# Kernel optimization log

Hardware: AMD Instinct MI355X
Metric: run time of the kernel (lower is better)

The kernel has to match this reference:

```python
import jax, jax.numpy as jnp
import numpy as np

NF, NH1, NH21, NH22, NCLS = 6, 128, 128, 128, 3
OBS_X, OBS_Y, OBS_Z, R = 10.0, 10.0, 9.0, 7.0
BATCH = 131072


def setup_inputs() -> dict:
    key = jax.random.key(0)
    ks = jax.random.split(key, 16)
    def lin(kw, kb, fan_in, fan_out):
        bound = 1.0 / np.sqrt(fan_in)
        w = jax.random.uniform(kw, (fan_out, fan_in), jnp.float32, -bound, bound)
        b = jax.random.uniform(kb, (fan_out,), jnp.float32, -bound, bound)
        return w, b
    fc1_w, fc1_b = lin(ks[0], ks[1], NF, NH1)
    fc21_w, fc21_b = lin(ks[2], ks[3], NH1, NH21)
    fc22_w, fc22_b = lin(ks[4], ks[5], NH1, NH22)
    fcm1_w, fcm1_b = lin(ks[6], ks[7], NH21, NH21)
    fcm2_w, fcm2_b = lin(ks[8], ks[9], NH22, NH22)
    fc31_w, fc31_b = lin(ks[10], ks[11], NH21, NCLS)
    fc32_w, fc32_b = lin(ks[12], ks[13], NH22, 2)
    x = jax.random.normal(ks[14], (BATCH, NF), jnp.float32)
    mean = jnp.array([10.0, 0.0, 10.0, 0.0, 9.0, 0.0], jnp.float32)
    std = jnp.array([5.0, 2.0, 5.0, 2.0, 5.0, 2.0], jnp.float32)
    return {"x": x, "mean": mean, "std": std,
            "fc1_w": fc1_w, "fc1_b": fc1_b,
            "fc21_w": fc21_w, "fc21_b": fc21_b,
            "fc22_w": fc22_w, "fc22_b": fc22_b,
            "fcm1_w": fcm1_w, "fcm1_b": fcm1_b,
            "fcm2_w": fcm2_w, "fcm2_b": fcm2_b,
            "fc31_w": fc31_w, "fc31_b": fc31_b,
            "fc32_w": fc32_w, "fc32_b": fc32_b,
            "sgn": 1}


def _forward(x, mean, std, fc1_w, fc1_b, fc21_w, fc21_b, fc22_w, fc22_b,
             fcm1_w, fcm1_b, fcm2_w, fcm2_b, fc31_w, fc31_b, fc32_w, fc32_b):
    x0 = x * std + mean                                   # de-normalized state [B,6]
    h = jnp.tanh(x @ fc1_w.T + fc1_b)                     # [B,NH1]
    x21 = jnp.tanh(h @ fc21_w.T + fc21_b)
    x22 = jnp.tanh(h @ fc22_w.T + fc22_b)
    x21 = jnp.tanh(x21 @ fcm1_w.T + fcm1_b)
    x22 = jnp.tanh(x22 @ fcm2_w.T + fcm2_b)
    x31 = x21 @ fc31_w.T + fc31_b                         # QP linear term p, [B,3]
    x32 = 4.0 * jax.nn.sigmoid(x22 @ fc32_w.T + fc32_b)   # HOCBF penalties, [B,2]

    # higher-order CBF terms
    px, vx, py, vy, pz, vz = (x0[:, i] for i in range(6))
    dx, dy, dz = px - OBS_X, py - OBS_Y, pz - OBS_Z
    barrier = dx**4 + dy**4 + dz**4 - R**4
    barrier_dot = 4.0 * (dx**3 * vx + dy**3 * vy + dz**3 * vz)
    Lf2b = 12.0 * (dx**2 * vx**2 + dy**2 * vy**2 + dz**2 * vz**2)
    G = -4.0 * jnp.stack([dx**3, dy**3, dz**3], axis=-1)  # [B,3], single constraint G u <= h
    hvec = Lf2b + (x32[:, 0] + x32[:, 1]) * barrier_dot + x32[:, 0] * x32[:, 1] * barrier  # [B]

    # QP: min 0.5 u^T u + x31^T u  s.t.  G u <= h  (Q = I, one constraint)
    # Closed-form KKT: u = -x31 - lam*G, lam = max(0, (G @ (-x31) - h) / (G @ G))
    u_unc = -x31
    Gu = jnp.sum(G * u_unc, axis=-1)                      # [B]
    GG = jnp.sum(G * G, axis=-1)                          # [B]
    lam = jnp.maximum(Gu - hvec, 0.0) / GG
    u = u_unc - lam[:, None] * G                          # [B,3]
    return u


def reference(x, mean, std, fc1_w, fc1_b, fc21_w, fc21_b, fc22_w, fc22_b,
              fcm1_w, fcm1_b, fcm2_w, fcm2_b, fc31_w, fc31_b, fc32_w, fc32_b, sgn):
    return _forward(x, mean, std, fc1_w, fc1_b, fc21_w, fc21_b, fc22_w, fc22_b,
                    fcm1_w, fcm1_b, fcm2_w, fcm2_b, fc31_w, fc31_b, fc32_w, fc32_b)
```

## Files before the change

kernel.cpp:

```cpp
#include <hip/hip_runtime.h>

typedef _Float16 half8 __attribute__((ext_vector_type(8)));
typedef _Float16 half4_t __attribute__((ext_vector_type(4)));
typedef __fp16 fp16x2 __attribute__((ext_vector_type(2)));
typedef float float4_t __attribute__((ext_vector_type(4)));
typedef float float2_t __attribute__((ext_vector_type(2)));

#define SB 64
#define NT 512
#define RS (SB * 8)

#define OFF_W1   0
#define OFF_W21  4096
#define OFF_W22  20480
#define OFF_WM1  36864
#define OFF_WM2  53248
#define OFF_W4A  69632
#define OFF_BIAS 73728
#define WS_HELEMS 73728

#define SCL_TANH 2.8853900817779268f
#define SCL_SIG  -1.4426950408889634f

__device__ __forceinline__ float tanh_pre(float a) {
  float e = __builtin_amdgcn_exp2f(a);
  return fmaf(-2.f, __builtin_amdgcn_rcpf(1.f + e), 1.f);
}
__device__ __forceinline__ half4_t pack4(float v0, float v1, float v2, float v3) {
  fp16x2 lo = __builtin_amdgcn_cvt_pkrtz(v0, v1);
  fp16x2 hi = __builtin_amdgcn_cvt_pkrtz(v2, v3);
  half4_t h;
  h[0] = (_Float16)lo[0]; h[1] = (_Float16)lo[1];
  h[2] = (_Float16)hi[0]; h[3] = (_Float16)hi[1];
  return h;
}

__global__ void prepack(const float* __restrict__ w1, const float* __restrict__ w21,
                        const float* __restrict__ w22, const float* __restrict__ wm1,
                        const float* __restrict__ wm2, const float* __restrict__ w31,
                        const float* __restrict__ w32, const float* __restrict__ b1,
                        const float* __restrict__ b21, const float* __restrict__ b22,
                        const float* __restrict__ bm1, const float* __restrict__ bm2,
                        _Float16* __restrict__ ws) {
  const int stride = gridDim.x * blockDim.x;
  for (int i = blockIdx.x * blockDim.x + threadIdx.x; i < WS_HELEMS; i += stride) {
    float v;
    if (i < OFF_W21) {
      int t = i;
      int j = t & 7, c = t >> 3, l16 = c & 15, t1 = c >> 4;
      int k8 = t1 & 3, mt = t1 >> 2;
      int row = mt * 16 + l16, k = k8 * 8 + j;
      v = (k < 6) ? w1[row * 6 + k] * SCL_TANH : 0.f;
    } else if (i < OFF_W4A) {
      int t = i - OFF_W21;
      int m = t >> 14; t &= 16383;
      const float* src = (m == 0) ? w21 : (m == 1) ? w22 : (m == 2) ? wm1 : wm2;
      int j = t & 7, c = t >> 3, l16 = c & 15, t1 = c >> 4;
      int k8 = t1 & 15, mt = t1 >> 4;
      v = src[(mt * 16 + l16) * 128 + k8 * 8 + j] * SCL_TANH;
    } else {
      int t = i - OFF_W4A;
      int j = t & 7, r = t >> 3, l16 = r & 15, q = r >> 4;
      int cc = q & 15, chain = q >> 4;
      int k = cc * 8 + j, m = l16;
      if (chain == 0) v = (m < 3) ? w31[m * 128 + k] : 0.f;
      else            v = (m < 2) ? w32[m * 128 + k] * SCL_SIG : 0.f;
    }
    ws[i] = (_Float16)v;
  }
  float* bws = (float*)(ws + OFF_BIAS);
  for (int i = blockIdx.x * blockDim.x + threadIdx.x; i < 640; i += stride) {
    int layer = i >> 7, idx = i & 127;
    const float* src = (layer == 0) ? b1 : (layer == 1) ? b21
                     : (layer == 2) ? b22 : (layer == 3) ? bm1 : bm2;
    bws[i] = src[idx] * SCL_TANH;
  }
}

__device__ __forceinline__ void layer128(const half8* __restrict__ A, float4_t bv,
                                         const _Float16* __restrict__ inB,
                                         _Float16* __restrict__ outB,
                                         int quad, int l16, int wv) {
  float4_t acc[4];
  acc[0] = bv; acc[1] = bv; acc[2] = bv; acc[3] = bv;
#pragma unroll
  for (int kk = 0; kk < 4; ++kk) {
#pragma unroll
    for (int nt = 0; nt < 4; ++nt) {
      half8 b = *(const half8*)(inB + (kk * 4 + quad) * RS + (nt * 16 + l16) * 8);
      acc[nt] = __builtin_amdgcn_mfma_f32_16x16x32_f16(A[kk], b, acc[nt], 0, 0, 0);
    }
  }
  const int ob = wv * 16 + quad * 4;
  _Float16* base = outB + (ob >> 3) * RS + (ob & 7);
#pragma unroll
  for (int nt = 0; nt < 4; ++nt) {
    const int s = nt * 16 + l16;
    half4_t h = pack4(tanh_pre(acc[nt][0]), tanh_pre(acc[nt][1]),
                      tanh_pre(acc[nt][2]), tanh_pre(acc[nt][3]));
    *(half4_t*)(base + s * 8) = h;
  }
}

__global__ __launch_bounds__(NT, 4) void bnet_main(
    const float* __restrict__ x, const float* __restrict__ meang,
    const float* __restrict__ stdg, const float* __restrict__ b31,
    const float* __restrict__ b32, const _Float16* __restrict__ ws,
    float* __restrict__ out) {
  __shared__ __align__(16) _Float16 bufH[SB * 128];
  __shared__ __align__(16) _Float16 bufA[SB * 128];
  __shared__ __align__(16) _Float16 bufB[SB * 128];

  const int tid = threadIdx.x;
  const int wv = tid >> 6;
  const int lane = tid & 63;
  const int quad = lane >> 4;
  const int l16 = lane & 15;
  const int s0 = blockIdx.x * SB;
  const float* biasF = (const float*)(ws + OFF_BIAS);
  const int arow = (wv * 16 + quad * 4);

  half8 A1 = *(const half8*)(ws + OFF_W1 + ((wv * 4 + quad) * 16 + l16) * 8);
  float4_t bv1 = *(const float4_t*)(biasF + arow);
  float4_t bv21 = *(const float4_t*)(biasF + 128 + arow);
  float4_t bv22 = *(const float4_t*)(biasF + 256 + arow);
  float4_t bvm1 = *(const float4_t*)(biasF + 384 + arow);
  float4_t bvm2 = *(const float4_t*)(biasF + 512 + arow);
  half8 A21[4];
#pragma unroll
  for (int kk = 0; kk < 4; ++kk)
    A21[kk] = *(const half8*)(ws + OFF_W21 + ((wv * 16 + kk * 4 + quad) * 16 + l16) * 8);

  {
    float4_t acc[4];
    acc[0] = bv1; acc[1] = bv1; acc[2] = bv1; acc[3] = bv1;
#pragma unroll
    for (int nt = 0; nt < 4; ++nt) {
      half8 v;
#pragma unroll
      for (int j = 0; j < 8; ++j) v[j] = (_Float16)0.f;
      if (quad == 0) {
        const float* xp = x + (size_t)(s0 + nt * 16 + l16) * 6;
        float2_t e0 = *(const float2_t*)(xp);
        float2_t e1 = *(const float2_t*)(xp + 2);
        float2_t e2 = *(const float2_t*)(xp + 4);
        v[0] = (_Float16)e0[0]; v[1] = (_Float16)e0[1];
        v[2] = (_Float16)e1[0]; v[3] = (_Float16)e1[1];
        v[4] = (_Float16)e2[0]; v[5] = (_Float16)e2[1];
      }
      acc[nt] = __builtin_amdgcn_mfma_f32_16x16x32_f16(A1, v, acc[nt], 0, 0, 0);
    }
    _Float16* base = bufH + (arow >> 3) * RS + (arow & 7);
#pragma unroll
    for (int nt = 0; nt < 4; ++nt) {
      const int s = nt * 16 + l16;
      half4_t h = pack4(tanh_pre(acc[nt][0]), tanh_pre(acc[nt][1]),
                        tanh_pre(acc[nt][2]), tanh_pre(acc[nt][3]));
      *(half4_t*)(base + s * 8) = h;
    }
  }
  half8 A22[4];
#pragma unroll
  for (int kk = 0; kk < 4; ++kk)
    A22[kk] = *(const half8*)(ws + OFF_W22 + ((wv * 16 + kk * 4 + quad) * 16 + l16) * 8);
  __syncthreads();

  layer128(A21, bv21, bufH, bufA, quad, l16, wv);
  half8 AM1[4];
#pragma unroll
  for (int kk = 0; kk < 4; ++kk)
    AM1[kk] = *(const half8*)(ws + OFF_WM1 + ((wv * 16 + kk * 4 + quad) * 16 + l16) * 8);
  layer128(A22, bv22, bufH, bufB, quad, l16, wv);
  __syncthreads();

  layer128(AM1, bvm1, bufA, bufH, quad, l16, wv);
  half8 AM2[4];
#pragma unroll
  for (int kk = 0; kk < 4; ++kk)
    AM2[kk] = *(const half8*)(ws + OFF_WM2 + ((wv * 16 + kk * 4 + quad) * 16 + l16) * 8);
  half8 A4[2][4];
  if (wv < 4) {
#pragma unroll
    for (int c = 0; c < 2; ++c)
#pragma unroll
      for (int kk = 0; kk < 4; ++kk)
        A4[c][kk] = *(const half8*)(ws + OFF_W4A +
                                    ((c * 16 + kk * 4 + quad) * 16 + l16) * 8);
  }
  __syncthreads();

  layer128(AM2, bvm2, bufB, bufA, quad, l16, wv);
  float4_t c0 = (float4_t){0.f, 0.f, 0.f, 0.f};
  if (wv < 4) {
    if (quad == 0) { c0[0] = b31[0]; c0[1] = b31[1]; c0[2] = b31[2]; }
    const int nt = wv;
#pragma unroll
    for (int kk = 0; kk < 4; ++kk) {
      half8 bh = *(const half8*)(bufH + (kk * 4 + quad) * RS + (nt * 16 + l16) * 8);
      c0 = __builtin_amdgcn_mfma_f32_16x16x32_f16(A4[0][kk], bh, c0, 0, 0, 0);
    }
  }
  __syncthreads();

  if (wv < 4) {
    const int nt = wv;
    float4_t c1 = (float4_t){0.f, 0.f, 0.f, 0.f};
    if (quad == 0) { c1[0] = b32[0] * SCL_SIG; c1[1] = b32[1] * SCL_SIG; }
#pragma unroll
    for (int kk = 0; kk < 4; ++kk) {
      half8 bc = *(const half8*)(bufA + (kk * 4 + quad) * RS + (nt * 16 + l16) * 8);
      c1 = __builtin_amdgcn_mfma_f32_16x16x32_f16(A4[1][kk], bc, c1, 0, 0, 0);
    }
    if (quad == 0) {
      const int s = nt * 16 + l16;
      float u0 = -c0[0];
      float u1 = -c0[1];
      float u2 = -c0[2];
      float p0 = 4.f * __builtin_amdgcn_rcpf(1.f + __builtin_amdgcn_exp2f(c1[0]));
      float p1 = 4.f * __builtin_amdgcn_rcpf(1.f + __builtin_amdgcn_exp2f(c1[1]));
      const float m0 = meang[0], m1 = meang[1], m2 = meang[2];
      const float m3 = meang[3], m4 = meang[4], m5 = meang[5];
      const float sd0 = stdg[0], sd1 = stdg[1], sd2 = stdg[2];
      const float sd3 = stdg[3], sd4 = stdg[4], sd5 = stdg[5];
      const float* xp = x + (size_t)(s0 + s) * 6;
      float2_t e0 = *(const float2_t*)(xp);
      float2_t e1 = *(const float2_t*)(xp + 2);
      float2_t e2 = *(const float2_t*)(xp + 4);
      float px = e0[0] * sd0 + m0, vx = e0[1] * sd1 + m1;
      float py = e1[0] * sd2 + m2, vy = e1[1] * sd3 + m3;
      float pz = e2[0] * sd4 + m4, vz = e2[1] * sd5 + m5;
      float dx = px - 10.f, dy = py - 10.f, dz = pz - 9.f;
      float dx2 = dx * dx, dy2 = dy * dy, dz2 = dz * dz;
      float dx3 = dx2 * dx, dy3 = dy2 * dy, dz3 = dz2 * dz;
      float barrier = dx3 * dx + dy3 * dy + dz3 * dz - 2401.f;
      float bdot = 4.f * (dx3 * vx + dy3 * vy + dz3 * vz);
      float Lf2b = 12.f * (dx2 * vx * vx + dy2 * vy * vy + dz2 * vz * vz);
      float g0 = -4.f * dx3, g1 = -4.f * dy3, g2 = -4.f * dz3;
      float hv = Lf2b + (p0 + p1) * bdot + p0 * p1 * barrier;
      float Gu = g0 * u0 + g1 * u1 + g2 * u2;
      float GG = g0 * g0 + g1 * g1 + g2 * g2;
      float lam = fmaxf(Gu - hv, 0.f) / GG;
      float* op = out + (size_t)(s0 + s) * 3;
      op[0] = u0 - lam * g0;
      op[1] = u1 - lam * g1;
      op[2] = u2 - lam * g2;
    }
  }
}

extern "C" void kernel_launch(void* const* d_in, const int* in_sizes, int n_in,
                              void* d_out, int out_size, void* d_ws, size_t ws_size,
                              hipStream_t stream) {
  const float* x    = (const float*)d_in[0];
  const float* mean = (const float*)d_in[1];
  const float* stdv = (const float*)d_in[2];
  const float* w1   = (const float*)d_in[3];
  const float* b1   = (const float*)d_in[4];
  const float* w21  = (const float*)d_in[5];
  const float* b21  = (const float*)d_in[6];
  const float* w22  = (const float*)d_in[7];
  const float* b22  = (const float*)d_in[8];
  const float* wm1  = (const float*)d_in[9];
  const float* bm1  = (const float*)d_in[10];
  const float* wm2  = (const float*)d_in[11];
  const float* bm2  = (const float*)d_in[12];
  const float* w31  = (const float*)d_in[13];
  const float* b31  = (const float*)d_in[14];
  const float* w32  = (const float*)d_in[15];
  const float* b32  = (const float*)d_in[16];
  _Float16* ws = (_Float16*)d_ws;
  float* out = (float*)d_out;
  const int batch = in_sizes[0] / 6;

  hipLaunchKernelGGL(prepack, dim3(96), dim3(256), 0, stream,
                     w1, w21, w22, wm1, wm2, w31, w32,
                     b1, b21, b22, bm1, bm2, ws);
  hipLaunchKernelGGL(bnet_main, dim3(batch / SB), dim3(NT), 0, stream,
                     x, mean, stdv, b31, b32, (const _Float16*)ws, out);
}
```

Measured before the change: 120.9 us.

## Switch hidden layers to 32x32x16 MFMA tiles and fuse fc21/fc22 passes

Rewrites the hidden-layer matmuls to use 32x32x16 MFMA instructions. Each wave now owns a 32-row output tile over 32 samples instead of 16 rows over all 64 samples, and the weight prepack layout is changed to match. The fc21 and fc22 layers now share each LDS B-fragment load inside one loop. The aim is fewer LDS reads per MFMA and higher MFMA efficiency, at the cost of more live registers (16-float accumulators and two sets of 8 A fragments held at once), which may hurt occupancy.

```diff
diff --git a/kernel.cpp b/kernel.cpp
--- a/kernel.cpp
+++ b/kernel.cpp
@@ -5,6 +5,7 @@
 typedef __fp16 fp16x2 __attribute__((ext_vector_type(2)));
 typedef float float4_t __attribute__((ext_vector_type(4)));
 typedef float float2_t __attribute__((ext_vector_type(2)));
+typedef float float16_t __attribute__((ext_vector_type(16)));
 
 #define SB 64
 #define NT 512
@@ -46,26 +47,25 @@
   for (int i = blockIdx.x * blockDim.x + threadIdx.x; i < WS_HELEMS; i += stride) {
     float v;
     if (i < OFF_W21) {
-      int t = i;
-      int j = t & 7, c = t >> 3, l16 = c & 15, t1 = c >> 4;
-      int k8 = t1 & 3, mt = t1 >> 2;
-      int row = mt * 16 + l16, k = k8 * 8 + j;
+      int j = i & 7, c = i >> 3, m32 = c & 31, t1 = c >> 5;
+      int half = t1 & 1, t2 = t1 >> 1, kc = t2 & 1, mt = t2 >> 1;
+      int row = mt * 32 + m32, k = kc * 16 + half * 8 + j;
       v = (k < 6) ? w1[row * 6 + k] * SCL_TANH : 0.f;
     } else if (i < OFF_W4A) {
       int t = i - OFF_W21;
       int m = t >> 14; t &= 16383;
       const float* src = (m == 0) ? w21 : (m == 1) ? w22 : (m == 2) ? wm1 : wm2;
-      int j = t & 7, c = t >> 3, l16 = c & 15, t1 = c >> 4;
-      int k8 = t1 & 15, mt = t1 >> 4;
-      v = src[(mt * 16 + l16) * 128 + k8 * 8 + j] * SCL_TANH;
-    } else {
+      int j = t & 7, c = t >> 3, m32 = c & 31, t1 = c >> 5;
+      int half = t1 & 1, t2 = t1 >> 1, kc = t2 & 7, mt = t2 >> 3;
+      v = src[(mt * 32 + m32) * 128 + kc * 16 + half * 8 + j] * SCL_TANH;
+    } else if (i < OFF_BIAS) {
       int t = i - OFF_W4A;
       int j = t & 7, r = t >> 3, l16 = r & 15, q = r >> 4;
       int cc = q & 15, chain = q >> 4;
       int k = cc * 8 + j, m = l16;
       if (chain == 0) v = (m < 3) ? w31[m * 128 + k] : 0.f;
       else            v = (m < 2) ? w32[m * 128 + k] * SCL_SIG : 0.f;
-    }
+    } else { v = 0.f; }
     ws[i] = (_Float16)v;
   }
   float* bws = (float*)(ws + OFF_BIAS);
@@ -77,29 +77,45 @@
   }
 }
 
-__device__ __forceinline__ void layer128(const half8* __restrict__ A, float4_t bv,
-                                         const _Float16* __restrict__ inB,
-                                         _Float16* __restrict__ outB,
-                                         int quad, int l16, int wv) {
-  float4_t acc[4];
-  acc[0] = bv; acc[1] = bv; acc[2] = bv; acc[3] = bv;
-#pragma unroll
-  for (int kk = 0; kk < 4; ++kk) {
-#pragma unroll
-    for (int nt = 0; nt < 4; ++nt) {
-      half8 b = *(const half8*)(inB + (kk * 4 + quad) * RS + (nt * 16 + l16) * 8);
-      acc[nt] = __builtin_amdgcn_mfma_f32_16x16x32_f16(A[kk], b, acc[nt], 0, 0, 0);
-    }
-  }
-  const int ob = wv * 16 + quad * 4;
-  _Float16* base = outB + (ob >> 3) * RS + (ob & 7);
-#pragma unroll
-  for (int nt = 0; nt < 4; ++nt) {
-    const int s = nt * 16 + l16;
-    half4_t h = pack4(tanh_pre(acc[nt][0]), tanh_pre(acc[nt][1]),
-                      tanh_pre(acc[nt][2]), tanh_pre(acc[nt][3]));
-    *(half4_t*)(base + s * 8) = h;
-  }
+template <int KC>
+__device__ __forceinline__ void loadA32(half8* A, const _Float16* base,
+                                        int mt, int half, int m32) {
+#pragma unroll
+  for (int kc = 0; kc < KC; ++kc)
+    A[kc] = *(const half8*)(base + (((mt * KC + kc) * 2 + half) * 32 + m32) * 8);
+}
+
+__device__ __forceinline__ float16_t bias_init32(const float* biasL, int mt, int half) {
+  float16_t a;
+#pragma unroll
+  for (int G = 0; G < 4; ++G) {
+    float4_t bv = *(const float4_t*)(biasL + mt * 32 + G * 8 + 4 * half);
+#pragma unroll
+    for (int i2 = 0; i2 < 4; ++i2) a[G * 4 + i2] = bv[i2];
+  }
+  return a;
+}
+
+__device__ __forceinline__ void store32(float16_t acc, _Float16* outB,
+                                        int mt, int half, int sOff) {
+#pragma unroll
+  for (int G = 0; G < 4; ++G) {
+    half4_t h = pack4(tanh_pre(acc[G * 4 + 0]), tanh_pre(acc[G * 4 + 1]),
+                      tanh_pre(acc[G * 4 + 2]), tanh_pre(acc[G * 4 + 3]));
+    *(half4_t*)(outB + (mt * 4 + G) * RS + sOff * 8 + 4 * half) = h;
+  }
+}
+
+__device__ __forceinline__ void pass32(const half8* A, const float* biasL,
+                                       const _Float16* inB, _Float16* outB,
+                                       int mt, int half, int sOff) {
+  float16_t acc = bias_init32(biasL, mt, half);
+#pragma unroll
+  for (int kc = 0; kc < 8; ++kc) {
+    half8 b = *(const half8*)(inB + (kc * 2 + half) * RS + sOff * 8);
+    acc = __builtin_amdgcn_mfma_f32_32x32x16_f16(A[kc], b, acc, 0, 0, 0);
+  }
+  store32(acc, outB, mt, half, sOff);
 }
 
 __global__ __launch_bounds__(NT, 4) void bnet_main(
@@ -114,70 +130,59 @@
   const int tid = threadIdx.x;
   const int wv = tid >> 6;
   const int lane = tid & 63;
+  const int half = lane >> 5;
+  const int m32 = lane & 31;
+  const int mt = wv & 3;
+  const int sg = wv >> 2;
+  const int sOff = sg * 32 + m32;
   const int quad = lane >> 4;
   const int l16 = lane & 15;
   const int s0 = blockIdx.x * SB;
   const float* biasF = (const float*)(ws + OFF_BIAS);
-  const int arow = (wv * 16 + quad * 4);
-
-  half8 A1 = *(const half8*)(ws + OFF_W1 + ((wv * 4 + quad) * 16 + l16) * 8);
-  float4_t bv1 = *(const float4_t*)(biasF + arow);
-  float4_t bv21 = *(const float4_t*)(biasF + 128 + arow);
-  float4_t bv22 = *(const float4_t*)(biasF + 256 + arow);
-  float4_t bvm1 = *(const float4_t*)(biasF + 384 + arow);
-  float4_t bvm2 = *(const float4_t*)(biasF + 512 + arow);
-  half8 A21[4];
-#pragma unroll
-  for (int kk = 0; kk < 4; ++kk)
-    A21[kk] = *(const half8*)(ws + OFF_W21 + ((wv * 16 + kk * 4 + quad) * 16 + l16) * 8);
+
+  half8 A21[8], A22[8];
+  loadA32<8>(A21, ws + OFF_W21, mt, half, m32);
+  loadA32<8>(A22, ws + OFF_W22, mt, half, m32);
 
   {
-    float4_t acc[4];
-    acc[0] = bv1; acc[1] = bv1; acc[2] = bv1; acc[3] = bv1;
-#pragma unroll
-    for (int nt = 0; nt < 4; ++nt) {
-      half8 v;
-#pragma unroll
-      for (int j = 0; j < 8; ++j) v[j] = (_Float16)0.f;
-      if (quad == 0) {
-        const float* xp = x + (size_t)(s0 + nt * 16 + l16) * 6;
-        float2_t e0 = *(const float2_t*)(xp);
-        float2_t e1 = *(const float2_t*)(xp + 2);
-        float2_t e2 = *(const float2_t*)(xp + 4);
-        v[0] = (_Float16)e0[0]; v[1] = (_Float16)e0[1];
-        v[2] = (_Float16)e1[0]; v[3] = (_Float16)e1[1];
-        v[4] = (_Float16)e2[0]; v[5] = (_Float16)e2[1];
-      }
-      acc[nt] = __builtin_amdgcn_mfma_f32_16x16x32_f16(A1, v, acc[nt], 0, 0, 0);
-    }
-    _Float16* base = bufH + (arow >> 3) * RS + (arow & 7);
-#pragma unroll
-    for (int nt = 0; nt < 4; ++nt) {
-      const int s = nt * 16 + l16;
-      half4_t h = pack4(tanh_pre(acc[nt][0]), tanh_pre(acc[nt][1]),
-                        tanh_pre(acc[nt][2]), tanh_pre(acc[nt][3]));
-      *(half4_t*)(base + s * 8) = h;
-    }
-  }
-  half8 A22[4];
-#pragma unroll
-  for (int kk = 0; kk < 4; ++kk)
-    A22[kk] = *(const half8*)(ws + OFF_W22 + ((wv * 16 + kk * 4 + quad) * 16 + l16) * 8);
-  __syncthreads();
-
-  layer128(A21, bv21, bufH, bufA, quad, l16, wv);
-  half8 AM1[4];
-#pragma unroll
-  for (int kk = 0; kk < 4; ++kk)
-    AM1[kk] = *(const half8*)(ws + OFF_WM1 + ((wv * 16 + kk * 4 + quad) * 16 + l16) * 8);
-  layer128(A22, bv22, bufH, bufB, quad, l16, wv);
-  __syncthreads();
-
-  layer128(AM1, bvm1, bufA, bufH, quad, l16, wv);
-  half8 AM2[4];
-#pragma unroll
-  for (int kk = 0; kk < 4; ++kk)
-    AM2[kk] = *(const half8*)(ws + OFF_WM2 + ((wv * 16 + kk * 4 + quad) * 16 + l16) * 8);
+    float16_t acc = bias_init32(biasF, mt, half);
+    half8 v;
+#pragma unroll
+    for (int j = 0; j < 8; ++j) v[j] = (_Float16)0.f;
+    if (half == 0) {
+      const float* xp = x + (size_t)(s0 + sOff) * 6;
+      float2_t e0 = *(const float2_t*)(xp);
+      float2_t e1 = *(const float2_t*)(xp + 2);
+      float2_t e2 = *(const float2_t*)(xp + 4);
+      v[0] = (_Float16)e0[0]; v[1] = (_Float16)e0[1];
+      v[2] = (_Float16)e1[0]; v[3] = (_Float16)e1[1];
+      v[4] = (_Float16)e2[0]; v[5] = (_Float16)e2[1];
+    }
+    half8 A1 = *(const half8*)(ws + OFF_W1 + ((mt * 2 * 2 + half) * 32 + m32) * 8);
+    acc = __builtin_amdgcn_mfma_f32_32x32x16_f16(A1, v, acc, 0, 0, 0);
+    store32(acc, bufH, mt, half, sOff);
+  }
+  __syncthreads();
+
+  {
+    float16_t a1 = bias_init32(biasF + 128, mt, half);
+    float16_t a2 = bias_init32(biasF + 256, mt, half);
+#pragma unroll
+    for (int kc = 0; kc < 8; ++kc) {
+      half8 b = *(const half8*)(bufH + (kc * 2 + half) * RS + sOff * 8);
+      a1 = __builtin_amdgcn_mfma_f32_32x32x16_f16(A21[kc], b, a1, 0, 0, 0);
+      a2 = __builtin_amdgcn_mfma_f32_32x32x16_f16(A22[kc], b, a2, 0, 0, 0);
+    }
+    store32(a1, bufA, mt, half, sOff);
+    store32(a2, bufB, mt, half, sOff);
+  }
+  half8 AM1[8];
+  loadA32<8>(AM1, ws + OFF_WM1, mt, half, m32);
+  __syncthreads();
+
+  pass32(AM1, biasF + 384, bufA, bufH, mt, half, sOff);
+  half8 AM2[8];
+  loadA32<8>(AM2, ws + OFF_WM2, mt, half, m32);
   half8 A4[2][4];
   if (wv < 4) {
 #pragma unroll
@@ -189,7 +194,7 @@
   }
   __syncthreads();
 
-  layer128(AM2, bvm2, bufB, bufA, quad, l16, wv);
+  pass32(AM2, biasF + 512, bufB, bufA, mt, half, sOff);
   float4_t c0 = (float4_t){0.f, 0.f, 0.f, 0.f};
   if (wv < 4) {
     if (quad == 0) { c0[0] = b31[0]; c0[1] = b31[1]; c0[2] = b31[2]; }
```

Measured after the change: 127.9 us. 1.06x slower.
